# Kernel tuning notes

Measured on AMD Instinct MI355X. Metric: run time of the kernel, lower is better.

## Reference

```python
import jax, jax.numpy as jnp
import numpy as np

CUTOFF = 5.0
EPS = 1e-3  # keras BatchNormalization default epsilon
L = 3       # num_interactions
N = 100000
E = 1600000
H = 64
FIN = 16


def setup_inputs() -> dict:
    key = jax.random.key(0)
    ks = jax.random.split(key, 16)
    s = 0.1  # weight scale for numerical stability
    return {
        "x": jax.random.normal(ks[0], (N, FIN), jnp.float32),
        "edge_index": jax.random.randint(ks[1], (2, E), 0, N, jnp.int32),
        "distances": jax.random.uniform(ks[2], (E,), jnp.float32) * CUTOFF,
        "edge_attr": jax.random.normal(ks[3], (E, 1), jnp.float32),
        "emb_W": jax.random.normal(ks[4], (FIN, H), jnp.float32) * s,
        "emb_b": jnp.zeros((H,), jnp.float32),
        "fW1": jax.random.normal(ks[5], (L, 1, H), jnp.float32) * s,
        "fb1": jnp.zeros((L, H), jnp.float32),
        "fW2": jax.random.normal(ks[6], (L, H, H), jnp.float32) * s,
        "fb2": jnp.zeros((L, H), jnp.float32),
        "iW1": jax.random.normal(ks[7], (L, H, H), jnp.float32) * s,
        "ib1": jnp.zeros((L, H), jnp.float32),
        "iW2": jax.random.normal(ks[8], (L, H, H), jnp.float32) * s,
        "ib2": jnp.zeros((L, H), jnp.float32),
        "bn_gamma": jnp.ones((L, H), jnp.float32),
        "bn_beta": jnp.zeros((L, H), jnp.float32),
        "oW1": jax.random.normal(ks[9], (H, H // 2), jnp.float32) * s,
        "ob1": jnp.zeros((H // 2,), jnp.float32),
        "og1": jnp.ones((H // 2,), jnp.float32),
        "obt1": jnp.zeros((H // 2,), jnp.float32),
        "oW2": jax.random.normal(ks[10], (H // 2, H // 2), jnp.float32) * s,
        "ob2": jnp.zeros((H // 2,), jnp.float32),
        "og2": jnp.ones((H // 2,), jnp.float32),
        "obt2": jnp.zeros((H // 2,), jnp.float32),
        "fin_W": jax.random.normal(ks[11], (H // 2, 3), jnp.float32) * s,
        "fin_b": jnp.zeros((3,), jnp.float32),
    }


def reference(x, edge_index, distances, edge_attr,
              emb_W, emb_b, fW1, fb1, fW2, fb2,
              iW1, ib1, iW2, ib2, bn_gamma, bn_beta,
              oW1, ob1, og1, obt1, oW2, ob2, og2, obt2,
              fin_W, fin_b):
    n_nodes = x.shape[0]
    row, col = edge_index[0], edge_index[1]
    inv = 1.0 / jnp.sqrt(1.0 + EPS)  # BN inference with moving mean=0, var=1

    # shared edge-level quantities
    scaled = distances * (2.0 / CUTOFF) - 1.0                       # [E]
    cut = 0.5 * (jnp.cos(distances * np.pi / CUTOFF) + 1.0)
    cut = jnp.where(distances <= CUTOFF, cut, 0.0)                  # [E]

    h = x @ emb_W + emb_b                                           # [N,H]
    for l in range(L):
        # filter MLP: [E,1] -> [E,F]
        f = jnp.tanh(scaled[:, None] * fW1[l][0] + fb1[l]) @ fW2[l] + fb2[l]
        f = f * cut[:, None]
        # original: sum_F(neighbor[:,None,:] * f[:,:,None]) == neighbor * sum_F(f)
        fs = f.sum(-1)                                              # [E]
        msgs = h[col] * fs[:, None]                                 # [E,H] gather
        agg = jax.ops.segment_sum(msgs, row, num_segments=n_nodes)  # [N,H] scatter-add
        out = jax.nn.softplus(agg @ iW1[l] + ib1[l]) @ iW2[l] + ib2[l]
        out = out * inv * bn_gamma[l] + bn_beta[l]                  # BN (inference)
        h = h + out

    g = h.mean(axis=0)                                              # [H]
    g = jax.nn.softplus(g @ oW1 + ob1) * inv * og1 + obt1
    g = jax.nn.softplus(g @ oW2 + ob2) * inv * og2 + obt2
    return g @ fin_W + fin_b                                        # [3]
```

## Files before the change

### kernel.cpp

```cpp
#include <hip/hip_runtime.h>
#include <hip/hip_fp16.h>
#include <math.h>

#define CUTOFF 5.0f
#define H 64
#define FIN 16
#define NLAYERS 3
#define LUTN 2048
#define LUTSTRIDE 2052
#define ASTRIDE 72
#define PCHUNK 16
#define WPSMAX 3136
#define MEANB 256
#define SUBSC 4

#define BN_INV 0.999500374750f

typedef _Float16 h8 __attribute__((ext_vector_type(8)));
typedef _Float16 h2 __attribute__((ext_vector_type(2)));
typedef float f32x4 __attribute__((ext_vector_type(4)));

__device__ __forceinline__ float softplus_f(float x) {
    return fmaxf(x, 0.f) + __logf(1.f + __expf(-fabsf(x)));
}

__global__ __launch_bounds__(1024)
void k_pre(const float* __restrict__ x, const float* __restrict__ emb_W,
           const float* __restrict__ emb_b, _Float16* __restrict__ h0,
           const float* __restrict__ fW1, const float* __restrict__ fb1,
           const float* __restrict__ fW2, const float* __restrict__ fb2,
           const float* __restrict__ iW1, const float* __restrict__ iW2,
           const float* __restrict__ bn_g, const float* __restrict__ bn_b,
           const float* __restrict__ ib2, h8* __restrict__ Wsw,
           float* __restrict__ b2p, float* __restrict__ lut,
           const int* __restrict__ ei, unsigned int* __restrict__ cntP,
           unsigned char* __restrict__ rank8,
           int N, int E, int CHUNK, int TW, int WPS, int RS,
           int nbH, int nbE16) {
    __shared__ unsigned s_cnt[WPSMAX];
    __shared__ float swsum[64];
    __shared__ float sbsum;
    int b = blockIdx.x;
    int t = threadIdx.x;
    if (b < nbH) {
        int c = b % PCHUNK;
        int s = b / PCHUNK;
        int wlo = s * WPS;
        int whi = min(wlo + WPS, TW);
        int nw = whi - wlo;
        int rlo = wlo * 4, rhi = whi * 4;
        for (int i = t; i < nw; i += 1024) s_cnt[i] = 0;
        __syncthreads();
        int e0 = c * CHUNK;
        int e1 = min(e0 + CHUNK, E);
#define HPROC(EE, RR) do { \
        int _r = (RR); \
        if (_r >= rlo && _r < rhi) { \
            int lr = _r - rlo; \
            unsigned old = atomicAdd(&s_cnt[lr >> 2], 1u << ((lr & 3) * 8)); \
            rank8[EE] = (unsigned char)((old >> ((lr & 3) * 8)) & 255u); \
        } } while (0)
        if (e0 < e1) {
            int nv = (e1 - e0) >> 2;
            const int4* ei4 = (const int4*)(ei + e0);
            for (int i = t; i < nv; i += 1024) {
                int4 r4 = ei4[i];
                int eb = e0 + 4 * i;
                HPROC(eb + 0, r4.x);
                HPROC(eb + 1, r4.y);
                HPROC(eb + 2, r4.z);
                HPROC(eb + 3, r4.w);
            }
            for (int e = e0 + 4 * nv + t; e < e1; e += 1024)
                HPROC(e, ei[e]);
        }
#undef HPROC
        __syncthreads();
        for (int i = t; i < nw; i += 1024)
            cntP[(size_t)c * TW + wlo + i] = s_cnt[i];
    } else if (b < nbH + nbE16) {
        int lane = t & 63;
        int w = t >> 6;
        int node = (b - nbH) * 16 + w;
        if (node < N) {
            float acc = emb_b[lane];
#pragma unroll
            for (int k = 0; k < FIN; k++) acc += x[node * FIN + k] * emb_W[k * H + lane];
            h0[(size_t)node * H + lane] = (_Float16)acc;
        }
    } else if (b < nbH + nbE16 + NLAYERS * 3) {
        int lb = b - nbH - nbE16;
        int l = lb / 3, part = lb % 3;
        if (t < 64) {
            float s = 0.f;
            for (int j = 0; j < H; j++) s += fW2[l * H * H + t * H + j];
            swsum[t] = s;
        }
        if (t == 64) {
            float s = 0.f;
            for (int j = 0; j < H; j++) s += fb2[l * H + j];
            sbsum = s;
        }
        __syncthreads();
        int i = part * 1024 + t;
        if (i <= LUTN) {
            float d = (float)i * (CUTOFF / (float)LUTN);
            float scaled = d * (2.0f / CUTOFF) - 1.0f;
            float cut = 0.5f * (__cosf(d * (3.14159265358979f / CUTOFF)) + 1.0f);
            if (d > CUTOFF) cut = 0.f;
            float s = 0.f;
            for (int hh = 0; hh < H; hh++) {
                int wi = l * H + hh;
                s += tanhf(scaled * fW1[wi] + fb1[wi]) * swsum[hh];
            }
            lut[l * LUTSTRIDE + i] = cut * (s + sbsum);
        }
    } else {
        int tid = (b - nbH - nbE16 - NLAYERS * 3) * 1024 + t;
        if (tid < NLAYERS * H)
            b2p[tid] = ib2[tid] * BN_INV * bn_g[tid] + bn_b[tid];
        if (tid < NLAYERS * 2 * 8 * 64) {
            int lane = tid & 63;
            int frag = (tid >> 6) & 7;
            int mat  = (tid >> 9) & 1;
            int l    = tid >> 10;
            int kt = frag >> 2, nt = frag & 3;
            int n = nt * 16 + (lane & 15);
            int k0 = kt * 32 + (lane >> 4) * 8;
            const float* W = (mat ? iW2 : iW1) + l * H * H;
            float scale = mat ? BN_INV * bn_g[l * H + n] : 1.0f;
            h8 v;
#pragma unroll
            for (int j = 0; j < 8; j++) v[j] = (_Float16)(W[(k0 + j) * H + n] * scale);
            Wsw[tid] = v;
        }
    }
}

__global__ void k_scan1(const unsigned int* __restrict__ cntP, int* __restrict__ bsums,
                        int N, int TW) {
    __shared__ int sd[256];
    int i = blockIdx.x * 256 + threadIdx.x;
    int v = 0;
    if (i < N) {
        int wi = i >> 2, sh = (i & 3) * 8;
#pragma unroll
        for (int p = 0; p < PCHUNK; p++)
            v += (int)((cntP[(size_t)p * TW + wi] >> sh) & 255u);
    }
    sd[threadIdx.x] = v;
    __syncthreads();
    for (int off = 128; off > 0; off >>= 1) {
        if (threadIdx.x < off) sd[threadIdx.x] += sd[threadIdx.x + off];
        __syncthreads();
    }
    if (threadIdx.x == 0) bsums[blockIdx.x] = sd[0];
}

__global__ void k_scan23(const unsigned int* __restrict__ cntP, const int* __restrict__ bsums,
                         int* __restrict__ row_ptr, int* __restrict__ base,
                         int N, int nb, int TW) {
    __shared__ int sd[256];
    __shared__ int ex[512];
    int t = threadIdx.x;
    int a0 = (2 * t     < nb) ? bsums[2 * t]     : 0;
    int a1 = (2 * t + 1 < nb) ? bsums[2 * t + 1] : 0;
    sd[t] = a0 + a1;
    __syncthreads();
    for (int off = 1; off < 256; off <<= 1) {
        int v = (t >= off) ? sd[t - off] : 0;
        __syncthreads();
        sd[t] += v;
        __syncthreads();
    }
    int pairExcl = (t == 0) ? 0 : sd[t - 1];
    ex[2 * t] = pairExcl;
    ex[2 * t + 1] = pairExcl + a0;
    __syncthreads();
    int myBase = ex[blockIdx.x];
    __syncthreads();

    int i = blockIdx.x * 256 + t;
    int c[PCHUNK];
    int v = 0;
    if (i < N) {
        int wi = i >> 2, sh = (i & 3) * 8;
#pragma unroll
        for (int p = 0; p < PCHUNK; p++) {
            c[p] = (int)((cntP[(size_t)p * TW + wi] >> sh) & 255u);
            v += c[p];
        }
    }
    sd[t] = v;
    __syncthreads();
    for (int off = 1; off < 256; off <<= 1) {
        int u = (t >= off) ? sd[t - off] : 0;
        __syncthreads();
        sd[t] += u;
        __syncthreads();
    }
    int excl = sd[t] - v + myBase;
    if (i < N) {
        row_ptr[i] = excl;
        int run = excl;
#pragma unroll
        for (int p = 0; p < PCHUNK; p++) { base[(size_t)p * N + i] = run; run += c[p]; }
        if (i == N - 1) row_ptr[N] = excl + v;
    }
}

__global__ __launch_bounds__(1024)
void k_scatter2(const int* __restrict__ ei, const float* __restrict__ dist,
                const unsigned char* __restrict__ rank8, const int* __restrict__ base,
                unsigned int* __restrict__ recs, int N, int E,
                int CHUNK, int WPS, int RS) {
    int b = blockIdx.x;
    int grp = PCHUNK * RS;
    int sub = b / grp;
    int r = b % grp;
    int c = r / RS, s = r % RS;
    int rlo = s * WPS * 4;
    int rhi = min(rlo + WPS * 4, N);
    int csub = CHUNK / SUBSC;
    int e0 = c * CHUNK + sub * csub;
    int e1 = min(e0 + csub, E);

#define SPROC(EE, RR) do { \
        int _r = (RR); \
        if (_r >= rlo && _r < rhi) { \
            int _e = (EE); \
            int col = ei[E + _e]; \
            float d = dist[_e]; \
            int didx = (int)(d * (32768.0f / CUTOFF) + 0.5f); \
            didx = max(0, min(didx, 32767)); \
            int pos = base[(size_t)c * N + _r] + (int)rank8[_e]; \
            recs[pos] = ((unsigned)col << 15) | (unsigned)didx; \
        } } while (0)
    if (e0 < e1) {
        int nv = (e1 - e0) >> 2;
        const int4* ei4 = (const int4*)(ei + e0);
        for (int i = threadIdx.x; i < nv; i += 1024) {
            int4 r4 = ei4[i];
            int eb = e0 + 4 * i;
            SPROC(eb + 0, r4.x);
            SPROC(eb + 1, r4.y);
            SPROC(eb + 2, r4.z);
            SPROC(eb + 3, r4.w);
        }
        for (int e = e0 + 4 * nv + (int)threadIdx.x; e < e1; e += 1024)
            SPROC(e, ei[e]);
    }
#undef SPROC
}

__global__ __launch_bounds__(256, 8)
void k_layer(const int* __restrict__ row_ptr, const unsigned int* __restrict__ recs,
             const float* __restrict__ lutl, const h8* __restrict__ Wsw,
             const float* __restrict__ b1, const float* __restrict__ b2p,
             const _Float16* __restrict__ h_in, _Float16* __restrict__ h_out,
             int N) {
    __shared__ float s_lut[LUTN + 1];
    __shared__ _Float16 sA[64 * ASTRIDE];
    for (int i = threadIdx.x; i <= LUTN; i += 256) s_lut[i] = lutl[i];
    __syncthreads();

    int lane = threadIdx.x & 63;
    int w = threadIdx.x >> 6;
    int base = blockIdx.x * 64 + w * 16;
    int g = lane >> 3, ci = lane & 7;
    const uint4* h4 = (const uint4*)h_in;

#pragma unroll
    for (int half = 0; half < 2; half++) {
        int node = base + half * 8 + g;
        h2 acc[4];
#pragma unroll
        for (int q = 0; q < 4; q++) acc[q] = (h2){(_Float16)0.f, (_Float16)0.f};
        if (node < N) {
            int s = row_ptr[node], t = row_ptr[node + 1];
            for (int k = s; k < t; k += 4) {
                int k1 = (k + 1 < t) ? k + 1 : k;
                int k2 = (k + 2 < t) ? k + 2 : k;
                int k3 = (k + 3 < t) ? k + 3 : k;
                unsigned r0 = recs[k];
                unsigned r1 = recs[k1];
                unsigned r2 = recs[k2];
                unsigned r3 = recs[k3];
                float td0 = (float)(r0 & 32767u) * (1.0f / 16.0f);
                float td1 = (float)(r1 & 32767u) * (1.0f / 16.0f);
                float td2 = (float)(r2 & 32767u) * (1.0f / 16.0f);
                float td3 = (float)(r3 & 32767u) * (1.0f / 16.0f);
                int i0 = (int)td0, i1 = (int)td1, i2 = (int)td2, i3 = (int)td3;
                float fr0 = td0 - (float)i0, fr1 = td1 - (float)i1;
                float fr2 = td2 - (float)i2, fr3 = td3 - (float)i3;
                float f00 = s_lut[i0], f01 = s_lut[i1];
                float f02 = s_lut[i2], f03 = s_lut[i3];
                float fv0 = f00 + fr0 * (s_lut[i0 + 1] - f00);
                float fv1 = f01 + fr1 * (s_lut[i1 + 1] - f01);
                float fv2 = f02 + fr2 * (s_lut[i2 + 1] - f02);
                float fv3 = f03 + fr3 * (s_lut[i3 + 1] - f03);
                fv1 = (k + 1 < t) ? fv1 : 0.f;
                fv2 = (k + 2 < t) ? fv2 : 0.f;
                fv3 = (k + 3 < t) ? fv3 : 0.f;
                union { uint4 u; h2 v[4]; } p0, p1, p2, p3;
                p0.u = h4[(r0 >> 15) * 8u + (unsigned)ci];
                p1.u = h4[(r1 >> 15) * 8u + (unsigned)ci];
                p2.u = h4[(r2 >> 15) * 8u + (unsigned)ci];
                p3.u = h4[(r3 >> 15) * 8u + (unsigned)ci];
                _Float16 fh0 = (_Float16)fv0, fh1 = (_Float16)fv1;
                _Float16 fh2 = (_Float16)fv2, fh3 = (_Float16)fv3;
                h2 a0 = (h2){fh0, fh0};
                h2 a1 = (h2){fh1, fh1};
                h2 a2 = (h2){fh2, fh2};
                h2 a3 = (h2){fh3, fh3};
#pragma unroll
                for (int q = 0; q < 4; q++) acc[q] += a0 * p0.v[q];
#pragma unroll
                for (int q = 0; q < 4; q++) acc[q] += a1 * p1.v[q];
#pragma unroll
                for (int q = 0; q < 4; q++) acc[q] += a2 * p2.v[q];
#pragma unroll
                for (int q = 0; q < 4; q++) acc[q] += a3 * p3.v[q];
            }
        }
        union { uint4 u4; h2 v[4]; } pk;
#pragma unroll
        for (int q = 0; q < 4; q++) pk.v[q] = acc[q];
        *(uint4*)&sA[(size_t)(w * 16 + half * 8 + g) * ASTRIDE + ci * 8] = pk.u4;
    }

    int q4 = lane >> 4, c16 = lane & 15;
    int rowb = w * 16;
    const h8* WB1 = Wsw;
    const h8* WB2 = Wsw + 8 * 64;
    h8 A0 = *(const h8*)&sA[(size_t)(rowb + c16) * ASTRIDE + q4 * 8];
    h8 A1 = *(const h8*)&sA[(size_t)(rowb + c16) * ASTRIDE + 32 + q4 * 8];
    f32x4 C1[4];
#pragma unroll
    for (int nt = 0; nt < 4; nt++) {
        f32x4 c = {0.f, 0.f, 0.f, 0.f};
        c = __builtin_amdgcn_mfma_f32_16x16x32_f16(A0, WB1[nt * 64 + lane], c, 0, 0, 0);
        c = __builtin_amdgcn_mfma_f32_16x16x32_f16(A1, WB1[(4 + nt) * 64 + lane], c, 0, 0, 0);
        C1[nt] = c;
    }
#pragma unroll
    for (int nt = 0; nt < 4; nt++) {
        float bb = b1[nt * 16 + c16];
#pragma unroll
        for (int reg = 0; reg < 4; reg++) {
            float v = softplus_f(C1[nt][reg] + bb);
            sA[(size_t)(rowb + q4 * 4 + reg) * ASTRIDE + nt * 16 + c16] = (_Float16)v;
        }
    }
    h8 M0 = *(const h8*)&sA[(size_t)(rowb + c16) * ASTRIDE + q4 * 8];
    h8 M1 = *(const h8*)&sA[(size_t)(rowb + c16) * ASTRIDE + 32 + q4 * 8];
    f32x4 C2[4];
#pragma unroll
    for (int nt = 0; nt < 4; nt++) {
        f32x4 c = {0.f, 0.f, 0.f, 0.f};
        c = __builtin_amdgcn_mfma_f32_16x16x32_f16(M0, WB2[nt * 64 + lane], c, 0, 0, 0);
        c = __builtin_amdgcn_mfma_f32_16x16x32_f16(M1, WB2[(4 + nt) * 64 + lane], c, 0, 0, 0);
        C2[nt] = c;
    }
#pragma unroll
    for (int nt = 0; nt < 4; nt++) {
        float bb2 = b2p[nt * 16 + c16];
#pragma unroll
        for (int reg = 0; reg < 4; reg++) {
            int node = base + q4 * 4 + reg;
            if (node < N) {
                size_t idx = (size_t)node * H + nt * 16 + c16;
                float hn = (float)h_in[idx] + C2[nt][reg] + bb2;
                h_out[idx] = (_Float16)hn;
            }
        }
    }
}

__global__ __launch_bounds__(256)
void k_mean(const _Float16* __restrict__ hb, float* __restrict__ partials, int N) {
    __shared__ float s_r[4][H];
    int lane = threadIdx.x & 63;
    int w = threadIdx.x >> 6;
    int wg = blockIdx.x * 4 + w;
    int stride = gridDim.x * 4;
    float local = 0.f;
    for (int i = wg; i < N; i += stride) local += (float)hb[(size_t)i * H + lane];
    s_r[w][lane] = local;
    __syncthreads();
    if (w == 0) {
        float s = s_r[0][lane] + s_r[1][lane] + s_r[2][lane] + s_r[3][lane];
        partials[(size_t)blockIdx.x * H + lane] = s;
    }
}

__global__ __launch_bounds__(256)
void k_final(const float* __restrict__ partials, int N,
             const float* __restrict__ oW1, const float* __restrict__ ob1,
             const float* __restrict__ og1, const float* __restrict__ obt1,
             const float* __restrict__ oW2, const float* __restrict__ ob2,
             const float* __restrict__ og2, const float* __restrict__ obt2,
             const float* __restrict__ fin_W, const float* __restrict__ fin_b,
             float* __restrict__ out) {
    __shared__ float red[4][H];
    __shared__ float sg[H], su[H / 2], sv[H / 2];
    int t = threadIdx.x;
    int ch = t & 63, grp = t >> 6;
    float s = 0.f;
    for (int b = grp; b < MEANB; b += 4) s += partials[(size_t)b * H + ch];
    red[grp][ch] = s;
    __syncthreads();
    if (t < H) sg[t] = (red[0][t] + red[1][t] + red[2][t] + red[3][t]) / (float)N;
    __syncthreads();
    int j = t;
    if (j < H / 2) {
        float acc = ob1[j];
        for (int k = 0; k < H; k++) acc += sg[k] * oW1[k * (H / 2) + j];
        su[j] = softplus_f(acc) * BN_INV * og1[j] + obt1[j];
    }
    __syncthreads();
    if (j < H / 2) {
        float acc = ob2[j];
        for (int k = 0; k < H / 2; k++) acc += su[k] * oW2[k * (H / 2) + j];
        sv[j] = softplus_f(acc) * BN_INV * og2[j] + obt2[j];
    }
    __syncthreads();
    if (j < 3) {
        float acc = fin_b[j];
        for (int k = 0; k < H / 2; k++) acc += sv[k] * fin_W[k * 3 + j];
        out[j] = acc;
    }
}

extern "C" void kernel_launch(void* const* d_in, const int* in_sizes, int n_in,
                              void* d_out, int out_size, void* d_ws, size_t ws_size,
                              hipStream_t stream) {
    const float* x      = (const float*)d_in[0];
    const int*   ei     = (const int*)d_in[1];
    const float* dist   = (const float*)d_in[2];
    const float* emb_W  = (const float*)d_in[4];
    const float* emb_b  = (const float*)d_in[5];
    const float* fW1    = (const float*)d_in[6];
    const float* fb1    = (const float*)d_in[7];
    const float* fW2    = (const float*)d_in[8];
    const float* fb2    = (const float*)d_in[9];
    const float* iW1    = (const float*)d_in[10];
    const float* ib1    = (const float*)d_in[11];
    const float* iW2    = (const float*)d_in[12];
    const float* ib2    = (const float*)d_in[13];
    const float* bn_g   = (const float*)d_in[14];
    const float* bn_b   = (const float*)d_in[15];
    const float* oW1    = (const float*)d_in[16];
    const float* ob1    = (const float*)d_in[17];
    const float* og1    = (const float*)d_in[18];
    const float* obt1   = (const float*)d_in[19];
    const float* oW2    = (const float*)d_in[20];
    const float* ob2    = (const float*)d_in[21];
    const float* og2    = (const float*)d_in[22];
    const float* obt2   = (const float*)d_in[23];
    const float* fin_W  = (const float*)d_in[24];
    const float* fin_b  = (const float*)d_in[25];
    float* out = (float*)d_out;

    int N = in_sizes[0] / FIN;
    int E = in_sizes[2];
    int nb_scan = (N + 255) / 256;

    int TW = (N + 3) / 4;
    int RS = (TW + WPSMAX - 1) / WPSMAX;
    int WPS = (TW + RS - 1) / RS;
    int CHUNK = (((E + PCHUNK - 1) / PCHUNK) + 15) & ~15;

    float*  ws   = (float*)d_ws;
    _Float16* h0 = (_Float16*)ws;
    _Float16* h1 = h0 + (size_t)N * H;
    unsigned int* recs = (unsigned int*)(h1 + (size_t)N * H);
    h8*     Wsw  = (h8*)(recs + E);
    float*  lut  = (float*)(Wsw + NLAYERS * 2 * 8 * 64);
    float*  partials = lut + 3 * LUTSTRIDE;
    float*  b2p  = partials + MEANB * H;
    unsigned int* cntP = (unsigned int*)(b2p + NLAYERS * H);
    int*    basep = (int*)(cntP + (size_t)PCHUNK * TW);
    int*    row_ptr = basep + (size_t)PCHUNK * N;
    int*    bsums   = row_ptr + (N + 1);
    unsigned char* rank8 = (unsigned char*)(bsums + 512);

    int nbH = PCHUNK * RS;
    int nbE16 = (N + 15) / 16;
    int nb_pre = nbH + nbE16 + NLAYERS * 3 + 3;
    k_pre<<<nb_pre, 1024, 0, stream>>>(x, emb_W, emb_b, h0,
                                       fW1, fb1, fW2, fb2, iW1, iW2,
                                       bn_g, bn_b, ib2, Wsw, b2p, lut,
                                       ei, cntP, rank8,
                                       N, E, CHUNK, TW, WPS, RS, nbH, nbE16);

    k_scan1<<<nb_scan, 256, 0, stream>>>(cntP, bsums, N, TW);
    k_scan23<<<nb_scan, 256, 0, stream>>>(cntP, bsums, row_ptr, basep, N, nb_scan, TW);

    k_scatter2<<<SUBSC * PCHUNK * RS, 1024, 0, stream>>>(ei, dist, rank8, basep,
                                                         recs, N, E, CHUNK, WPS, RS);

    _Float16* hp[2] = {h0, h1};
    int nb_tile = (N + 63) / 64;
    for (int l = 0; l < NLAYERS; l++) {
        k_layer<<<nb_tile, 256, 0, stream>>>(row_ptr, recs, lut + (size_t)l * LUTSTRIDE,
                                             Wsw + (size_t)l * 1024,
                                             ib1 + l * H, b2p + l * H,
                                             hp[l & 1], hp[(l + 1) & 1], N);
    }
    _Float16* h_final = hp[NLAYERS & 1];

    k_mean<<<MEANB, 256, 0, stream>>>(h_final, partials, N);
    k_final<<<1, 256, 0, stream>>>(partials, N, oW1, ob1, og1, obt1,
                                   oW2, ob2, og2, obt2, fin_W, fin_b, out);
}
```

Before: 367.5 us.

## Replace rank-based CSR scatter with two-pass bucketed binning through staging buffer

After: 348.0 us. -5.3%, faster.

```diff
diff --git a/kernel.cpp b/kernel.cpp
--- a/kernel.cpp
+++ b/kernel.cpp
@@ -12,13 +12,17 @@
 #define PCHUNK 16
 #define WPSMAX 3136
 #define MEANB 256
-#define SUBSC 4
+#define BROWS 512
+#define NBMAX 256
+#define MAXC 10240
+#define ABLK 4096
 
 #define BN_INV 0.999500374750f
 
 typedef _Float16 h8 __attribute__((ext_vector_type(8)));
 typedef _Float16 h2 __attribute__((ext_vector_type(2)));
 typedef float f32x4 __attribute__((ext_vector_type(4)));
+typedef unsigned int u32x2 __attribute__((ext_vector_type(2)));
 
 __device__ __forceinline__ float softplus_f(float x) {
     return fmaxf(x, 0.f) + __logf(1.f + __expf(-fabsf(x)));
@@ -34,7 +38,6 @@
            const float* __restrict__ ib2, h8* __restrict__ Wsw,
            float* __restrict__ b2p, float* __restrict__ lut,
            const int* __restrict__ ei, unsigned int* __restrict__ cntP,
-           unsigned char* __restrict__ rank8,
            int N, int E, int CHUNK, int TW, int WPS, int RS,
            int nbH, int nbE16) {
     __shared__ unsigned s_cnt[WPSMAX];
@@ -53,26 +56,24 @@
         __syncthreads();
         int e0 = c * CHUNK;
         int e1 = min(e0 + CHUNK, E);
-#define HPROC(EE, RR) do { \
+#define HPROC(RR) do { \
         int _r = (RR); \
         if (_r >= rlo && _r < rhi) { \
             int lr = _r - rlo; \
-            unsigned old = atomicAdd(&s_cnt[lr >> 2], 1u << ((lr & 3) * 8)); \
-            rank8[EE] = (unsigned char)((old >> ((lr & 3) * 8)) & 255u); \
+            atomicAdd(&s_cnt[lr >> 2], 1u << ((lr & 3) * 8)); \
         } } while (0)
         if (e0 < e1) {
             int nv = (e1 - e0) >> 2;
             const int4* ei4 = (const int4*)(ei + e0);
             for (int i = t; i < nv; i += 1024) {
                 int4 r4 = ei4[i];
-                int eb = e0 + 4 * i;
-                HPROC(eb + 0, r4.x);
-                HPROC(eb + 1, r4.y);
-                HPROC(eb + 2, r4.z);
-                HPROC(eb + 3, r4.w);
+                HPROC(r4.x);
+                HPROC(r4.y);
+                HPROC(r4.z);
+                HPROC(r4.w);
             }
             for (int e = e0 + 4 * nv + t; e < e1; e += 1024)
-                HPROC(e, ei[e]);
+                HPROC(ei[e]);
         }
 #undef HPROC
         __syncthreads();
@@ -158,7 +159,7 @@
 }
 
 __global__ void k_scan23(const unsigned int* __restrict__ cntP, const int* __restrict__ bsums,
-                         int* __restrict__ row_ptr, int* __restrict__ base,
+                         int* __restrict__ row_ptr, unsigned int* __restrict__ cursor,
                          int N, int nb, int TW) {
     __shared__ int sd[256];
     __shared__ int ex[512];
@@ -181,15 +182,12 @@
     __syncthreads();
 
     int i = blockIdx.x * 256 + t;
-    int c[PCHUNK];
     int v = 0;
     if (i < N) {
         int wi = i >> 2, sh = (i & 3) * 8;
 #pragma unroll
-        for (int p = 0; p < PCHUNK; p++) {
-            c[p] = (int)((cntP[(size_t)p * TW + wi] >> sh) & 255u);
-            v += c[p];
-        }
+        for (int p = 0; p < PCHUNK; p++)
+            v += (int)((cntP[(size_t)p * TW + wi] >> sh) & 255u);
     }
     sd[t] = v;
     __syncthreads();
@@ -202,55 +200,84 @@
     int excl = sd[t] - v + myBase;
     if (i < N) {
         row_ptr[i] = excl;
-        int run = excl;
-#pragma unroll
-        for (int p = 0; p < PCHUNK; p++) { base[(size_t)p * N + i] = run; run += c[p]; }
+        if ((i & (BROWS - 1)) == 0) cursor[i / BROWS] = (unsigned)excl;
         if (i == N - 1) row_ptr[N] = excl + v;
     }
 }
 
 __global__ __launch_bounds__(1024)
-void k_scatter2(const int* __restrict__ ei, const float* __restrict__ dist,
-                const unsigned char* __restrict__ rank8, const int* __restrict__ base,
-                unsigned int* __restrict__ recs, int N, int E,
-                int CHUNK, int WPS, int RS) {
-    int b = blockIdx.x;
-    int grp = PCHUNK * RS;
-    int sub = b / grp;
-    int r = b % grp;
-    int c = r / RS, s = r % RS;
-    int rlo = s * WPS * 4;
-    int rhi = min(rlo + WPS * 4, N);
-    int csub = CHUNK / SUBSC;
-    int e0 = c * CHUNK + sub * csub;
-    int e1 = min(e0 + csub, E);
-
-#define SPROC(EE, RR) do { \
-        int _r = (RR); \
-        if (_r >= rlo && _r < rhi) { \
-            int _e = (EE); \
-            int col = ei[E + _e]; \
-            float d = dist[_e]; \
-            int didx = (int)(d * (32768.0f / CUTOFF) + 0.5f); \
-            didx = max(0, min(didx, 32767)); \
-            int pos = base[(size_t)c * N + _r] + (int)rank8[_e]; \
-            recs[pos] = ((unsigned)col << 15) | (unsigned)didx; \
-        } } while (0)
-    if (e0 < e1) {
-        int nv = (e1 - e0) >> 2;
-        const int4* ei4 = (const int4*)(ei + e0);
-        for (int i = threadIdx.x; i < nv; i += 1024) {
-            int4 r4 = ei4[i];
-            int eb = e0 + 4 * i;
-            SPROC(eb + 0, r4.x);
-            SPROC(eb + 1, r4.y);
-            SPROC(eb + 2, r4.z);
-            SPROC(eb + 3, r4.w);
-        }
-        for (int e = e0 + 4 * nv + (int)threadIdx.x; e < e1; e += 1024)
-            SPROC(e, ei[e]);
-    }
-#undef SPROC
+void k_passA(const int* __restrict__ ei, const float* __restrict__ dist,
+             unsigned int* __restrict__ cursor, u32x2* __restrict__ stg,
+             int N, int E, int NB) {
+    __shared__ unsigned s_cnt[NBMAX];
+    __shared__ unsigned s_base[NBMAX];
+    int t = threadIdx.x;
+    int e0 = blockIdx.x * ABLK;
+    for (int i = t; i < NB; i += 1024) s_cnt[i] = 0;
+    __syncthreads();
+    int rowv[4];
+    unsigned rkv[4] = {0u, 0u, 0u, 0u};
+    int bkv[4] = {0, 0, 0, 0};
+#pragma unroll
+    for (int j = 0; j < 4; j++) {
+        int e = e0 + j * 1024 + t;
+        rowv[j] = -1;
+        if (e < E) {
+            int r = ei[e];
+            int bk = r / BROWS;
+            rkv[j] = atomicAdd(&s_cnt[bk], 1u);
+            bkv[j] = bk;
+            rowv[j] = r;
+        }
+    }
+    __syncthreads();
+    for (int i = t; i < NB; i += 1024)
+        s_base[i] = s_cnt[i] ? atomicAdd(&cursor[i], s_cnt[i]) : 0u;
+    __syncthreads();
+#pragma unroll
+    for (int j = 0; j < 4; j++) {
+        int e = e0 + j * 1024 + t;
+        if (e < E) {
+            int col = ei[E + e];
+            float d = dist[e];
+            int didx = (int)(d * (32768.0f / CUTOFF) + 0.5f);
+            didx = max(0, min(didx, 32767));
+            u32x2 rec;
+            rec.x = ((unsigned)col << 15) | (unsigned)didx;
+            rec.y = (unsigned)rowv[j];
+            stg[s_base[bkv[j]] + rkv[j]] = rec;
+        }
+    }
+}
+
+__global__ __launch_bounds__(1024)
+void k_passB(const u32x2* __restrict__ stg, const int* __restrict__ row_ptr,
+             unsigned int* __restrict__ recs, int N) {
+    __shared__ int s_ptr[BROWS];
+    __shared__ unsigned s_out[MAXC];
+    int b = blockIdx.x, t = threadIdx.x;
+    int r0 = b * BROWS;
+    int r1 = min(r0 + BROWS, N);
+    int p0 = row_ptr[r0];
+    int p1 = row_ptr[r1];
+    int cnt = p1 - p0;
+    for (int i = t; i < r1 - r0; i += 1024) s_ptr[i] = row_ptr[r0 + i] - p0;
+    __syncthreads();
+    if (cnt <= MAXC) {
+        for (int i = t; i < cnt; i += 1024) {
+            u32x2 rec = stg[p0 + i];
+            int slot = atomicAdd(&s_ptr[(int)rec.y - r0], 1);
+            s_out[slot] = rec.x;
+        }
+        __syncthreads();
+        for (int i = t; i < cnt; i += 1024) recs[p0 + i] = s_out[i];
+    } else {
+        for (int i = t; i < cnt; i += 1024) {
+            u32x2 rec = stg[p0 + i];
+            int slot = atomicAdd(&s_ptr[(int)rec.y - r0], 1);
+            recs[p0 + slot] = rec.x;
+        }
+    }
 }
 
 __global__ __launch_bounds__(256, 8)
@@ -470,6 +497,7 @@
     int RS = (TW + WPSMAX - 1) / WPSMAX;
     int WPS = (TW + RS - 1) / RS;
     int CHUNK = (((E + PCHUNK - 1) / PCHUNK) + 15) & ~15;
+    int NB = (N + BROWS - 1) / BROWS;
 
     float*  ws   = (float*)d_ws;
     _Float16* h0 = (_Float16*)ws;
@@ -479,11 +507,11 @@
     float*  lut  = (float*)(Wsw + NLAYERS * 2 * 8 * 64);
     float*  partials = lut + 3 * LUTSTRIDE;
     float*  b2p  = partials + MEANB * H;
-    unsigned int* cntP = (unsigned int*)(b2p + NLAYERS * H);
-    int*    basep = (int*)(cntP + (size_t)PCHUNK * TW);
-    int*    row_ptr = basep + (size_t)PCHUNK * N;
+    u32x2*  stg  = (u32x2*)(b2p + NLAYERS * H);
+    unsigned int* cntP = (unsigned int*)(stg + E);
+    int*    row_ptr = (int*)(cntP + (size_t)PCHUNK * TW);
     int*    bsums   = row_ptr + (N + 1);
-    unsigned char* rank8 = (unsigned char*)(bsums + 512);
+    unsigned int* cursor = (unsigned int*)(bsums + 512);
 
     int nbH = PCHUNK * RS;
     int nbE16 = (N + 15) / 16;
@@ -491,14 +519,15 @@
     k_pre<<<nb_pre, 1024, 0, stream>>>(x, emb_W, emb_b, h0,
                                        fW1, fb1, fW2, fb2, iW1, iW2,
                                        bn_g, bn_b, ib2, Wsw, b2p, lut,
-                                       ei, cntP, rank8,
+                                       ei, cntP,
                                        N, E, CHUNK, TW, WPS, RS, nbH, nbE16);
 
     k_scan1<<<nb_scan, 256, 0, stream>>>(cntP, bsums, N, TW);
-    k_scan23<<<nb_scan, 256, 0, stream>>>(cntP, bsums, row_ptr, basep, N, nb_scan, TW);
-
-    k_scatter2<<<SUBSC * PCHUNK * RS, 1024, 0, stream>>>(ei, dist, rank8, basep,
-                                                         recs, N, E, CHUNK, WPS, RS);
+    k_scan23<<<nb_scan, 256, 0, stream>>>(cntP, bsums, row_ptr, cursor, N, nb_scan, TW);
+
+    int nbA = (E + ABLK - 1) / ABLK;
+    k_passA<<<nbA, 1024, 0, stream>>>(ei, dist, cursor, stg, N, E, NB);
+    k_passB<<<NB, 1024, 0, stream>>>(stg, row_ptr, recs, N);
 
     _Float16* hp[2] = {h0, h1};
     int nb_tile = (N + 63) / 64;
```
